# Optimization experiments

Hardware: AMD Instinct MI355X
Metric: run time of the kernel (lower is better)

The kernel has to match this reference:

```python
import jax, jax.numpy as jnp
import numpy as np

N = 131072  # B*L nodes
H = 256     # hidden_dim


def setup_inputs() -> dict:
    key = jax.random.key(0)
    ks = jax.random.split(key, 13)
    s = 0.02
    return {
        "h": jax.random.normal(ks[0], (N, H), jnp.float32),
        "pos": jax.random.normal(ks[1], (N, 3), jnp.float32),
        # edge_mlp: Linear(2H+1 -> H), SiLU, Linear(H -> H)
        "ew1": jax.random.normal(ks[2], (2 * H + 1, H), jnp.float32) * s,
        "eb1": jnp.zeros((H,), jnp.float32),
        "ew2": jax.random.normal(ks[3], (H, H), jnp.float32) * s,
        "eb2": jnp.zeros((H,), jnp.float32),
        # pos_mlp: Linear(H -> H), SiLU, Linear(H -> 3, bias=False)
        "pw1": jax.random.normal(ks[4], (H, H), jnp.float32) * s,
        "pb1": jnp.zeros((H,), jnp.float32),
        "pw2": jax.random.normal(ks[5], (H, 3), jnp.float32) * s,
        # node_mlp: Linear(2H -> H), SiLU, Linear(H -> H)
        "nw1": jax.random.normal(ks[6], (2 * H, H), jnp.float32) * s,
        "nb1": jnp.zeros((H,), jnp.float32),
        "nw2": jax.random.normal(ks[7], (H, H), jnp.float32) * s,
        "nb2": jnp.zeros((H,), jnp.float32),
    }


def reference(h, pos, ew1, eb1, ew2, eb2, pw1, pb1, pw2, nw1, nb1, nw2, nb2):
    # Chain edges: row = 0..N-2, col = 1..N-1 -> slices instead of gathers.
    rel_pos = pos[1:] - pos[:-1]                                   # [N-1, 3]
    dist = jnp.linalg.norm(rel_pos, axis=-1, keepdims=True)        # [N-1, 1]
    edge_feat = jnp.concatenate([h[:-1], h[1:], dist], axis=-1)    # [N-1, 2H+1]
    edge_attr = jax.nn.silu(edge_feat @ ew1 + eb1) @ ew2 + eb2     # [N-1, H]
    delta_pos = jax.nn.silu(edge_attr @ pw1 + pb1) @ pw2           # [N-1, 3]

    hd = h.shape[1]
    z3 = jnp.zeros((1, 3), pos.dtype)
    zH = jnp.zeros((1, hd), h.dtype)
    # scatter-add over unique chain indices == padded shifts
    pos_update = jnp.concatenate([delta_pos, z3], 0) - jnp.concatenate([z3, delta_pos], 0)
    node_update = jnp.concatenate([edge_attr, zH], 0) + jnp.concatenate([zH, edge_attr], 0)

    h_cat = jnp.concatenate([h, node_update], axis=-1)             # [N, 2H]
    h_out = jax.nn.silu(h_cat @ nw1 + nb1) @ nw2 + nb2             # [N, H]
    pos_out = pos + 0.1 * pos_update                               # [N, 3]
    return h_out, pos_out
```

## Files before the change

kernel.cpp:

```cpp
#include <hip/hip_runtime.h>
#include <hip/hip_bf16.h>
#include <math.h>

#define NN 131072
#define HD 256

typedef __bf16 bf16;
typedef __attribute__((ext_vector_type(8))) __bf16 bf16x8;
typedef __attribute__((ext_vector_type(4))) __bf16 bf16x4;
typedef __attribute__((ext_vector_type(4))) float f32x4;

__device__ __forceinline__ float silu_f(float x) { return x / (1.f + __expf(-x)); }

__device__ __forceinline__ float bfu2f(unsigned int lo16) {
    unsigned int u = lo16 << 16;
    return __builtin_bit_cast(float, u);
}
__device__ __forceinline__ unsigned short f2bfu(float f) {
    bf16 b = (bf16)f;
    return __builtin_bit_cast(unsigned short, b);
}

template<int KSTEPS, int RN>
__device__ __forceinline__ void mm_tileR(const bf16* Xl, int bk0, const bf16x8* __restrict__ Bp,
                                         int wave, int lane, f32x4 acc[RN][4]) {
    const int lrow = lane & 15, lkhi = lane >> 4;
    #pragma unroll
    for (int ks = 0; ks < KSTEPS; ++ks) {
        bf16x8 a[RN];
        #pragma unroll
        for (int r = 0; r < RN; ++r)
            a[r] = *(const bf16x8*)&Xl[(r * 16 + lrow) * 264 + ks * 32 + lkhi * 8];
        #pragma unroll
        for (int c = 0; c < 4; ++c) {
            bf16x8 b = Bp[((bk0 + ks) * 16 + wave * 4 + c) * 64 + lane];
            #pragma unroll
            for (int r = 0; r < RN; ++r)
                acc[r][c] = __builtin_amdgcn_mfma_f32_16x16x32_bf16(a[r], b, acc[r][c], 0, 0, 0);
        }
    }
}

__device__ __forceinline__ void packW(const float* __restrict__ W, bf16* __restrict__ P, int idx) {
    int j  = idx & 7;
    int ln = (idx >> 3) & 63;
    int cb = (idx >> 9) & 15;
    int ks = idx >> 13;
    int k = ks * 32 + ((ln >> 4) << 3) + j;
    int n = (cb << 4) + (ln & 15);
    P[idx] = (bf16)W[k * HD + n];
}

__global__ void pack_kernel(const float* __restrict__ ew1, const float* __restrict__ ew2,
                            const float* __restrict__ pw1, const float* __restrict__ nw1,
                            const float* __restrict__ nw2,
                            bf16* __restrict__ ew1p, bf16* __restrict__ ew2p,
                            bf16* __restrict__ pw1p, bf16* __restrict__ nw1p,
                            bf16* __restrict__ nw2p) {
    int t = blockIdx.x * 256 + threadIdx.x;
    if (t < 131072) { packW(ew1, ew1p, t); return; }
    t -= 131072;
    if (t < 65536)  { packW(ew2, ew2p, t); return; }
    t -= 65536;
    if (t < 65536)  { packW(pw1, pw1p, t); return; }
    t -= 65536;
    if (t < 131072) { packW(nw1, nw1p, t); return; }
    t -= 131072;
    if (t < 65536)  { packW(nw2, nw2p, t); return; }
}

__global__ __launch_bounds__(256, 2) void edge_kernel(
    const float* __restrict__ h, const float* __restrict__ pos,
    const float* __restrict__ ew1, const float* __restrict__ eb1,
    const float* __restrict__ eb2, const float* __restrict__ pb1,
    const float* __restrict__ pw2,
    const bf16x8* __restrict__ ew1p, const bf16x8* __restrict__ ew2p,
    const bf16x8* __restrict__ pw1p, const bf16x8* __restrict__ nw1p,
    bf16* __restrict__ q1_g, uint2* __restrict__ p1_g,
    float* __restrict__ dp_g) {
    __shared__ bf16 X[129 * 264];
    __shared__ float dist_s[128];
    __shared__ float dp_s[4][128][3];

    const int tid = threadIdx.x;
    const int lane = tid & 63, wave = tid >> 6;
    const int lrow = lane & 15, lkhi = lane >> 4;
    const int e0 = blockIdx.x * 128;

    for (int idx = tid; idx < 129 * 64; idx += 256) {
        int r = idx >> 6, c4 = (idx & 63) << 2;
        int gr = e0 + r;
        float4 v = make_float4(0.f, 0.f, 0.f, 0.f);
        if (gr < NN) v = *(const float4*)&h[(size_t)gr * HD + c4];
        bf16x4 b;
        b[0] = (bf16)v.x; b[1] = (bf16)v.y; b[2] = (bf16)v.z; b[3] = (bf16)v.w;
        *(bf16x4*)&X[r * 264 + c4] = b;
    }
    if (tid < 128) {
        int e = e0 + tid;
        float d = 0.f;
        if (e < NN - 1) {
            float dx = pos[3 * e + 3] - pos[3 * e];
            float dy = pos[3 * e + 4] - pos[3 * e + 1];
            float dz = pos[3 * e + 5] - pos[3 * e + 2];
            d = sqrtf(dx * dx + dy * dy + dz * dz);
        }
        dist_s[tid] = d;
    }
    float bias1[4], bias2[4], bias3[4], wlast[4], w2l[4][3], b1n[4];
    #pragma unroll
    for (int c = 0; c < 4; ++c) {
        int col = (wave * 4 + c) * 16 + lrow;
        bias1[c] = eb1[col];
        bias2[c] = eb2[col];
        bias3[c] = pb1[col];
        wlast[c] = ew1[512 * HD + col];
        #pragma unroll
        for (int x = 0; x < 3; ++x) w2l[c][x] = pw2[col * 3 + x];
    }
    (void)b1n;
    __syncthreads();

    f32x4 acc[8][4];

    #pragma unroll
    for (int r = 0; r < 8; ++r)
        #pragma unroll
        for (int c = 0; c < 4; ++c) acc[r][c] = (f32x4)0.f;
    mm_tileR<8, 8>(X, 0, nw1p, wave, lane, acc);
    #pragma unroll
    for (int r = 0; r < 8; ++r) {
        size_t nb = (size_t)blockIdx.x * 2 + (r >> 2);
        uint2* p1w = p1_g + (nb * 4 + wave) * 1024;
        #pragma unroll
        for (int c = 0; c < 4; ++c) {
            uint2 v;
            v.x = (unsigned int)f2bfu(acc[r][c][0]) | ((unsigned int)f2bfu(acc[r][c][1]) << 16);
            v.y = (unsigned int)f2bfu(acc[r][c][2]) | ((unsigned int)f2bfu(acc[r][c][3]) << 16);
            p1w[(((r & 3) * 4 + c)) * 64 + lane] = v;
        }
    }

    #pragma unroll
    for (int r = 0; r < 8; ++r)
        #pragma unroll
        for (int c = 0; c < 4; ++c) acc[r][c] = (f32x4)0.f;
    #pragma unroll
    for (int ks = 0; ks < 16; ++ks) {
        const int rb = (ks >= 8) ? 1 : 0;
        const int kk = ks * 32 + lkhi * 8 - rb * 256;
        bf16x8 a[8];
        #pragma unroll
        for (int r = 0; r < 8; ++r)
            a[r] = *(const bf16x8*)&X[(r * 16 + lrow + rb) * 264 + kk];
        #pragma unroll
        for (int c = 0; c < 4; ++c) {
            bf16x8 b = ew1p[(ks * 16 + wave * 4 + c) * 64 + lane];
            #pragma unroll
            for (int r = 0; r < 8; ++r)
                acc[r][c] = __builtin_amdgcn_mfma_f32_16x16x32_bf16(a[r], b, acc[r][c], 0, 0, 0);
        }
    }
    __syncthreads();
    #pragma unroll
    for (int r = 0; r < 8; ++r)
        #pragma unroll
        for (int c = 0; c < 4; ++c)
            #pragma unroll
            for (int q = 0; q < 4; ++q) {
                int row = r * 16 + lkhi * 4 + q;
                int col = (wave * 4 + c) * 16 + lrow;
                float v = acc[r][c][q] + dist_s[row] * wlast[c] + bias1[c];
                X[row * 264 + col] = (bf16)silu_f(v);
            }
    __syncthreads();

    #pragma unroll
    for (int r = 0; r < 8; ++r)
        #pragma unroll
        for (int c = 0; c < 4; ++c) acc[r][c] = (f32x4)0.f;
    mm_tileR<8, 8>(X, 0, ew2p, wave, lane, acc);
    __syncthreads();
    #pragma unroll
    for (int r = 0; r < 8; ++r)
        #pragma unroll
        for (int c = 0; c < 4; ++c)
            #pragma unroll
            for (int q = 0; q < 4; ++q) {
                int row = r * 16 + lkhi * 4 + q;
                int col = (wave * 4 + c) * 16 + lrow;
                X[row * 264 + col] = (bf16)(acc[r][c][q] + bias2[c]);
            }
    __syncthreads();

    #pragma unroll
    for (int r = 0; r < 8; ++r)
        #pragma unroll
        for (int c = 0; c < 4; ++c) acc[r][c] = (f32x4)0.f;
    mm_tileR<8, 8>(X, 0, pw1p, wave, lane, acc);
    #pragma unroll
    for (int r = 0; r < 8; ++r) {
        float red[12];
        #pragma unroll
        for (int q = 0; q < 4; ++q) {
            float t3v[4];
            #pragma unroll
            for (int c = 0; c < 4; ++c) t3v[c] = silu_f(acc[r][c][q] + bias3[c]);
            #pragma unroll
            for (int x = 0; x < 3; ++x) {
                float s = 0.f;
                #pragma unroll
                for (int c = 0; c < 4; ++c) s += t3v[c] * w2l[c][x];
                red[q * 3 + x] = s;
            }
        }
        #pragma unroll
        for (int i = 0; i < 12; ++i) {
            float v = red[i];
            v += __shfl_xor(v, 1);
            v += __shfl_xor(v, 2);
            v += __shfl_xor(v, 4);
            v += __shfl_xor(v, 8);
            red[i] = v;
        }
        if (lrow == 0) {
            #pragma unroll
            for (int q = 0; q < 4; ++q)
                #pragma unroll
                for (int x = 0; x < 3; ++x)
                    dp_s[wave][r * 16 + lkhi * 4 + q][x] = red[q * 3 + x];
        }
    }

    #pragma unroll
    for (int r = 0; r < 8; ++r)
        #pragma unroll
        for (int c = 0; c < 4; ++c) acc[r][c] = (f32x4)0.f;
    mm_tileR<8, 8>(X, 8, nw1p, wave, lane, acc);

    __syncthreads();
    #pragma unroll
    for (int r = 0; r < 8; ++r)
        #pragma unroll
        for (int c = 0; c < 4; ++c)
            #pragma unroll
            for (int q = 0; q < 4; ++q) {
                int row = r * 16 + lkhi * 4 + q;
                int col = (wave * 4 + c) * 16 + lrow;
                X[row * 264 + col] = (bf16)acc[r][c][q];
            }
    for (int idx = tid; idx < 128 * 3; idx += 256) {
        int row = idx / 3, x = idx - row * 3;
        float s = dp_s[0][row][x] + dp_s[1][row][x] + dp_s[2][row][x] + dp_s[3][row][x];
        dp_g[(size_t)(e0 + row) * 3 + x] = s;
    }
    __syncthreads();
    for (int idx = tid; idx < 128 * 128; idx += 256) {
        int r = idx >> 7, cu = idx & 127;
        ((unsigned int*)&q1_g[(size_t)(e0 + r) * HD])[cu] = ((const unsigned int*)&X[r * 264])[cu];
    }
}

__global__ __launch_bounds__(256, 4) void node_kernel(
    const float* __restrict__ pos,
    const float* __restrict__ nb1, const float* __restrict__ nb2,
    const bf16x8* __restrict__ nw2p,
    const bf16* __restrict__ q1_g, const uint2* __restrict__ p1_g,
    const float* __restrict__ dp_g,
    float* __restrict__ h_out, float* __restrict__ pos_out) {
    __shared__ bf16 X[65 * 264];

    const int tid = threadIdx.x;
    const int lane = tid & 63, wave = tid >> 6;
    const int lrow = lane & 15, lkhi = lane >> 4;
    const int n0 = blockIdx.x * 64;

    if (tid < 192) {
        int row = tid & 63, col = tid >> 6;
        int i = n0 + row;
        float dpi = (i < NN - 1) ? dp_g[(size_t)i * 3 + col] : 0.f;
        float dpm = (i > 0) ? dp_g[(size_t)(i - 1) * 3 + col] : 0.f;
        pos_out[(size_t)i * 3 + col] = pos[(size_t)i * 3 + col] + 0.1f * (dpi - dpm);
    }

    for (int idx = tid; idx < 65 * 32; idx += 256) {
        int t = idx >> 5, cu = idx & 31;
        int er = n0 - 1 + t;
        uint4 v = make_uint4(0u, 0u, 0u, 0u);
        if (er >= 0 && er <= NN - 2) v = ((const uint4*)&q1_g[(size_t)er * HD])[cu];
        ((uint4*)&X[t * 264])[cu] = v;
    }
    uint2 p1r[16];
    {
        const uint2* p1p = p1_g + ((size_t)blockIdx.x * 4 + wave) * 1024;
        #pragma unroll
        for (int i = 0; i < 16; ++i) p1r[i] = p1p[i * 64 + lane];
    }
    float b1[4];
    #pragma unroll
    for (int c = 0; c < 4; ++c) b1[c] = nb1[(wave * 4 + c) * 16 + lrow];
    __syncthreads();

    unsigned int t4p[32];
    #pragma unroll
    for (int r = 0; r < 4; ++r)
        #pragma unroll
        for (int c = 0; c < 4; ++c) {
            int i = r * 4 + c;
            int col = (wave * 4 + c) * 16 + lrow;
            #pragma unroll
            for (int qh = 0; qh < 2; ++qh) {
                unsigned int pk = qh == 0 ? p1r[i].x : p1r[i].y;
                unsigned int outp = 0;
                #pragma unroll
                for (int j = 0; j < 2; ++j) {
                    int q = 2 * qh + j;
                    int row = r * 16 + lkhi * 4 + q;
                    float p1v = bfu2f(j == 0 ? (pk & 0xffffu) : (pk >> 16));
                    float z = p1v + (float)X[(row + 1) * 264 + col] + (float)X[row * 264 + col] + b1[c];
                    unsigned short tb = f2bfu(silu_f(z));
                    outp |= (unsigned int)tb << (16 * j);
                }
                t4p[i * 2 + qh] = outp;
            }
        }
    __syncthreads();
    #pragma unroll
    for (int r = 0; r < 4; ++r)
        #pragma unroll
        for (int c = 0; c < 4; ++c) {
            int i = r * 4 + c;
            int col = (wave * 4 + c) * 16 + lrow;
            #pragma unroll
            for (int q = 0; q < 4; ++q) {
                int row = r * 16 + lkhi * 4 + q;
                unsigned int pk = t4p[i * 2 + (q >> 1)];
                unsigned short tb = (unsigned short)((q & 1) ? (pk >> 16) : (pk & 0xffffu));
                X[row * 264 + col] = __builtin_bit_cast(bf16, tb);
            }
        }
    __syncthreads();

    f32x4 acc[4][4];
    #pragma unroll
    for (int r = 0; r < 4; ++r)
        #pragma unroll
        for (int c = 0; c < 4; ++c) acc[r][c] = (f32x4)0.f;
    mm_tileR<8, 4>(X, 0, nw2p, wave, lane, acc);
    float b2[4];
    #pragma unroll
    for (int c = 0; c < 4; ++c) b2[c] = nb2[(wave * 4 + c) * 16 + lrow];
    #pragma unroll
    for (int r = 0; r < 4; ++r)
        #pragma unroll
        for (int c = 0; c < 4; ++c)
            #pragma unroll
            for (int q = 0; q < 4; ++q) {
                int row = r * 16 + lkhi * 4 + q;
                int col = (wave * 4 + c) * 16 + lrow;
                h_out[(size_t)(n0 + row) * HD + col] = acc[r][c][q] + b2[c];
            }
}

extern "C" void kernel_launch(void* const* d_in, const int* in_sizes, int n_in,
                              void* d_out, int out_size, void* d_ws, size_t ws_size,
                              hipStream_t stream) {
    const float* h   = (const float*)d_in[0];
    const float* pos = (const float*)d_in[1];
    const float* ew1 = (const float*)d_in[2];
    const float* eb1 = (const float*)d_in[3];
    const float* ew2 = (const float*)d_in[4];
    const float* eb2 = (const float*)d_in[5];
    const float* pw1 = (const float*)d_in[6];
    const float* pb1 = (const float*)d_in[7];
    const float* pw2 = (const float*)d_in[8];
    const float* nw1 = (const float*)d_in[9];
    const float* nb1 = (const float*)d_in[10];
    const float* nw2 = (const float*)d_in[11];
    const float* nb2 = (const float*)d_in[12];

    char* ws = (char*)d_ws;
    bf16*  q1   = (bf16*)ws;
    float* dp   = (float*)(ws + 67108864);
    uint2* p1   = (uint2*)(ws + 68681728);
    char*  wsw = ws + 135790592;
    bf16*  ew1p = (bf16*)(wsw);
    bf16*  ew2p = (bf16*)(wsw + 262144);
    bf16*  pw1p = (bf16*)(wsw + 393216);
    bf16*  nw1p = (bf16*)(wsw + 524288);
    bf16*  nw2p = (bf16*)(wsw + 786432);

    float* out = (float*)d_out;
    float* h_out = out;
    float* pos_out = out + (size_t)NN * HD;

    pack_kernel<<<1792, 256, 0, stream>>>(ew1, ew2, pw1, nw1, nw2,
                                          ew1p, ew2p, pw1p, nw1p, nw2p);
    edge_kernel<<<1024, 256, 0, stream>>>(h, pos, ew1, eb1, eb2, pb1, pw2,
                                          (const bf16x8*)ew1p, (const bf16x8*)ew2p,
                                          (const bf16x8*)pw1p, (const bf16x8*)nw1p,
                                          q1, p1, dp);
    node_kernel<<<2048, 256, 0, stream>>>(pos, nb1, nb2,
                                          (const bf16x8*)nw2p,
                                          q1, (const uint2*)p1, dp, h_out, pos_out);
}
```

Measured before the change: 278.9 us.

## Fold biases and dist into extra MFMA k-step, prefetch weights, write q1 in fragment layout

Biases and the distance column are packed as extra K rows of the weight matrices, and a ones/dist vector in shared memory feeds one extra MFMA step, so the scalar bias and dist epilogue arithmetic goes away. Weight fragments are double-buffered one k-step ahead to hide global load latency. Some GEMMs swap their A/B operands so each lane's accumulator holds four consecutive columns, which allows packed 8-byte LDS stores. The q1 intermediate is written straight from registers in fragment layout instead of through shared memory, and the node kernel reads it back per lane including a halo row from the previous block. This adds more complex indexing, an extra MFMA step per GEMM, and bias rounding to bf16.

After: 276.5 us. Within noise of the previous version (-0.9%).

```diff
diff --git a/kernel.cpp b/kernel.cpp
--- a/kernel.cpp
+++ b/kernel.cpp
@@ -20,66 +20,111 @@
     bf16 b = (bf16)f;
     return __builtin_bit_cast(unsigned short, b);
 }
-
-template<int KSTEPS, int RN>
-__device__ __forceinline__ void mm_tileR(const bf16* Xl, int bk0, const bf16x8* __restrict__ Bp,
-                                         int wave, int lane, f32x4 acc[RN][4]) {
+__device__ __forceinline__ uint2 pack4(float a, float b, float c, float d) {
+    uint2 v;
+    v.x = (unsigned int)f2bfu(a) | ((unsigned int)f2bfu(b) << 16);
+    v.y = (unsigned int)f2bfu(c) | ((unsigned int)f2bfu(d) << 16);
+    return v;
+}
+
+template<int KS, bool SWAP>
+__device__ __forceinline__ void mmP(const bf16* Xl, int bk0, const bf16x8* __restrict__ Bp,
+                                    int wave, int lane, f32x4 acc[8][4]) {
     const int lrow = lane & 15, lkhi = lane >> 4;
-    #pragma unroll
-    for (int ks = 0; ks < KSTEPS; ++ks) {
-        bf16x8 a[RN];
-        #pragma unroll
-        for (int r = 0; r < RN; ++r)
+    bf16x8 bcur[4], bnxt[4];
+    #pragma unroll
+    for (int c = 0; c < 4; ++c)
+        bcur[c] = Bp[(bk0 * 16 + wave * 4 + c) * 64 + lane];
+    #pragma unroll
+    for (int ks = 0; ks < KS; ++ks) {
+        if (ks + 1 < KS) {
+            #pragma unroll
+            for (int c = 0; c < 4; ++c)
+                bnxt[c] = Bp[((bk0 + ks + 1) * 16 + wave * 4 + c) * 64 + lane];
+        }
+        bf16x8 a[8];
+        #pragma unroll
+        for (int r = 0; r < 8; ++r)
             a[r] = *(const bf16x8*)&Xl[(r * 16 + lrow) * 264 + ks * 32 + lkhi * 8];
         #pragma unroll
-        for (int c = 0; c < 4; ++c) {
-            bf16x8 b = Bp[((bk0 + ks) * 16 + wave * 4 + c) * 64 + lane];
-            #pragma unroll
-            for (int r = 0; r < RN; ++r)
-                acc[r][c] = __builtin_amdgcn_mfma_f32_16x16x32_bf16(a[r], b, acc[r][c], 0, 0, 0);
-        }
-    }
-}
-
-__device__ __forceinline__ void packW(const float* __restrict__ W, bf16* __restrict__ P, int idx) {
+        for (int c = 0; c < 4; ++c)
+            #pragma unroll
+            for (int r = 0; r < 8; ++r)
+                acc[r][c] = SWAP
+                    ? __builtin_amdgcn_mfma_f32_16x16x32_bf16(bcur[c], a[r], acc[r][c], 0, 0, 0)
+                    : __builtin_amdgcn_mfma_f32_16x16x32_bf16(a[r], bcur[c], acc[r][c], 0, 0, 0);
+        #pragma unroll
+        for (int c = 0; c < 4; ++c) bcur[c] = bnxt[c];
+    }
+}
+
+template<bool SWAP>
+__device__ __forceinline__ void extrasStep(const bf16* EXT, const bf16x8* __restrict__ Bp, int ksx,
+                                           int wave, int lane, f32x4 acc[8][4]) {
+    const int lrow = lane & 15, lkhi = lane >> 4;
+    bf16x8 bext[4];
+    #pragma unroll
+    for (int c = 0; c < 4; ++c)
+        bext[c] = Bp[(ksx * 16 + wave * 4 + c) * 64 + lane];
+    bf16x8 zero;
+    #pragma unroll
+    for (int j = 0; j < 8; ++j) zero[j] = (bf16)0.f;
+    #pragma unroll
+    for (int r = 0; r < 8; ++r) {
+        bf16x8 ae = (lkhi == 0) ? *(const bf16x8*)&EXT[(r * 16 + lrow) * 8] : zero;
+        #pragma unroll
+        for (int c = 0; c < 4; ++c)
+            acc[r][c] = SWAP
+                ? __builtin_amdgcn_mfma_f32_16x16x32_bf16(bext[c], ae, acc[r][c], 0, 0, 0)
+                : __builtin_amdgcn_mfma_f32_16x16x32_bf16(ae, bext[c], acc[r][c], 0, 0, 0);
+    }
+}
+
+__device__ __forceinline__ void packGen(const float* __restrict__ W, const float* __restrict__ bias,
+                                        const float* __restrict__ extra, int Kreal,
+                                        bf16* __restrict__ P, int idx) {
     int j  = idx & 7;
     int ln = (idx >> 3) & 63;
     int cb = (idx >> 9) & 15;
     int ks = idx >> 13;
     int k = ks * 32 + ((ln >> 4) << 3) + j;
     int n = (cb << 4) + (ln & 15);
-    P[idx] = (bf16)W[k * HD + n];
-}
-
-__global__ void pack_kernel(const float* __restrict__ ew1, const float* __restrict__ ew2,
-                            const float* __restrict__ pw1, const float* __restrict__ nw1,
-                            const float* __restrict__ nw2,
+    float v;
+    if (k < Kreal) v = W[k * HD + n];
+    else if (k == Kreal) v = bias ? bias[n] : 0.f;
+    else if (k == Kreal + 1) v = extra ? extra[n] : 0.f;
+    else v = 0.f;
+    P[idx] = (bf16)v;
+}
+
+__global__ void pack_kernel(const float* __restrict__ ew1, const float* __restrict__ eb1,
+                            const float* __restrict__ ew2, const float* __restrict__ eb2,
+                            const float* __restrict__ pw1, const float* __restrict__ pb1,
+                            const float* __restrict__ nw1, const float* __restrict__ nw2,
                             bf16* __restrict__ ew1p, bf16* __restrict__ ew2p,
                             bf16* __restrict__ pw1p, bf16* __restrict__ nw1p,
                             bf16* __restrict__ nw2p) {
     int t = blockIdx.x * 256 + threadIdx.x;
-    if (t < 131072) { packW(ew1, ew1p, t); return; }
+    if (t < 139264) { packGen(ew1, eb1, ew1 + 512 * HD, 512, ew1p, t); return; }
+    t -= 139264;
+    if (t < 73728)  { packGen(ew2, eb2, nullptr, 256, ew2p, t); return; }
+    t -= 73728;
+    if (t < 73728)  { packGen(pw1, pb1, nullptr, 256, pw1p, t); return; }
+    t -= 73728;
+    if (t < 131072) { packGen(nw1, nullptr, nullptr, 512, nw1p, t); return; }
     t -= 131072;
-    if (t < 65536)  { packW(ew2, ew2p, t); return; }
-    t -= 65536;
-    if (t < 65536)  { packW(pw1, pw1p, t); return; }
-    t -= 65536;
-    if (t < 131072) { packW(nw1, nw1p, t); return; }
-    t -= 131072;
-    if (t < 65536)  { packW(nw2, nw2p, t); return; }
+    if (t < 65536)  { packGen(nw2, nullptr, nullptr, 256, nw2p, t); return; }
 }
 
 __global__ __launch_bounds__(256, 2) void edge_kernel(
     const float* __restrict__ h, const float* __restrict__ pos,
-    const float* __restrict__ ew1, const float* __restrict__ eb1,
-    const float* __restrict__ eb2, const float* __restrict__ pb1,
     const float* __restrict__ pw2,
     const bf16x8* __restrict__ ew1p, const bf16x8* __restrict__ ew2p,
     const bf16x8* __restrict__ pw1p, const bf16x8* __restrict__ nw1p,
-    bf16* __restrict__ q1_g, uint2* __restrict__ p1_g,
+    uint2* __restrict__ q1f_g, uint2* __restrict__ p1_g,
     float* __restrict__ dp_g) {
     __shared__ bf16 X[129 * 264];
-    __shared__ float dist_s[128];
+    __shared__ bf16 EXT[128 * 8];
     __shared__ float dp_s[4][128][3];
 
     const int tid = threadIdx.x;
@@ -105,20 +150,19 @@
             float dz = pos[3 * e + 5] - pos[3 * e + 2];
             d = sqrtf(dx * dx + dy * dy + dz * dz);
         }
-        dist_s[tid] = d;
-    }
-    float bias1[4], bias2[4], bias3[4], wlast[4], w2l[4][3], b1n[4];
+        uint2 a, z;
+        a.x = (unsigned int)f2bfu(1.0f) | ((unsigned int)f2bfu(d) << 16);
+        a.y = 0u; z.x = 0u; z.y = 0u;
+        *(uint2*)&EXT[tid * 8] = a;
+        *(uint2*)&EXT[tid * 8 + 4] = z;
+    }
+    float w2l[4][3];
     #pragma unroll
     for (int c = 0; c < 4; ++c) {
-        int col = (wave * 4 + c) * 16 + lrow;
-        bias1[c] = eb1[col];
-        bias2[c] = eb2[col];
-        bias3[c] = pb1[col];
-        wlast[c] = ew1[512 * HD + col];
-        #pragma unroll
-        for (int x = 0; x < 3; ++x) w2l[c][x] = pw2[col * 3 + x];
-    }
-    (void)b1n;
+        int n = (wave * 4 + c) * 16 + lrow;
+        #pragma unroll
+        for (int x = 0; x < 3; ++x) w2l[c][x] = pw2[n * 3 + x];
+    }
     __syncthreads();
 
     f32x4 acc[8][4];
@@ -127,77 +171,86 @@
     for (int r = 0; r < 8; ++r)
         #pragma unroll
         for (int c = 0; c < 4; ++c) acc[r][c] = (f32x4)0.f;
-    mm_tileR<8, 8>(X, 0, nw1p, wave, lane, acc);
+    mmP<8, true>(X, 0, nw1p, wave, lane, acc);
     #pragma unroll
     for (int r = 0; r < 8; ++r) {
         size_t nb = (size_t)blockIdx.x * 2 + (r >> 2);
-        uint2* p1w = p1_g + (nb * 4 + wave) * 1024;
+        uint2* w = p1_g + (nb * 4 + wave) * 1024;
+        #pragma unroll
+        for (int c = 0; c < 4; ++c)
+            w[((r & 3) * 4 + c) * 64 + lane] =
+                pack4(acc[r][c][0], acc[r][c][1], acc[r][c][2], acc[r][c][3]);
+    }
+
+    #pragma unroll
+    for (int r = 0; r < 8; ++r)
+        #pragma unroll
+        for (int c = 0; c < 4; ++c) acc[r][c] = (f32x4)0.f;
+    {
+        bf16x8 bcur[4], bnxt[4];
+        #pragma unroll
+        for (int c = 0; c < 4; ++c)
+            bcur[c] = ew1p[(wave * 4 + c) * 64 + lane];
+        #pragma unroll
+        for (int ks = 0; ks < 16; ++ks) {
+            if (ks < 15) {
+                #pragma unroll
+                for (int c = 0; c < 4; ++c)
+                    bnxt[c] = ew1p[((ks + 1) * 16 + wave * 4 + c) * 64 + lane];
+            }
+            const int rb = (ks >= 8) ? 1 : 0;
+            const int kk = ks * 32 + lkhi * 8 - rb * 256;
+            bf16x8 a[8];
+            #pragma unroll
+            for (int r = 0; r < 8; ++r)
+                a[r] = *(const bf16x8*)&X[(r * 16 + lrow + rb) * 264 + kk];
+            #pragma unroll
+            for (int c = 0; c < 4; ++c)
+                #pragma unroll
+                for (int r = 0; r < 8; ++r)
+                    acc[r][c] = __builtin_amdgcn_mfma_f32_16x16x32_bf16(bcur[c], a[r], acc[r][c], 0, 0, 0);
+            #pragma unroll
+            for (int c = 0; c < 4; ++c) bcur[c] = bnxt[c];
+        }
+    }
+    extrasStep<true>(EXT, ew1p, 16, wave, lane, acc);
+    __syncthreads();
+    #pragma unroll
+    for (int r = 0; r < 8; ++r)
         #pragma unroll
         for (int c = 0; c < 4; ++c) {
-            uint2 v;
-            v.x = (unsigned int)f2bfu(acc[r][c][0]) | ((unsigned int)f2bfu(acc[r][c][1]) << 16);
-            v.y = (unsigned int)f2bfu(acc[r][c][2]) | ((unsigned int)f2bfu(acc[r][c][3]) << 16);
-            p1w[(((r & 3) * 4 + c)) * 64 + lane] = v;
-        }
-    }
-
-    #pragma unroll
-    for (int r = 0; r < 8; ++r)
-        #pragma unroll
-        for (int c = 0; c < 4; ++c) acc[r][c] = (f32x4)0.f;
-    #pragma unroll
-    for (int ks = 0; ks < 16; ++ks) {
-        const int rb = (ks >= 8) ? 1 : 0;
-        const int kk = ks * 32 + lkhi * 8 - rb * 256;
-        bf16x8 a[8];
-        #pragma unroll
-        for (int r = 0; r < 8; ++r)
-            a[r] = *(const bf16x8*)&X[(r * 16 + lrow + rb) * 264 + kk];
+            int m = 16 * r + lrow;
+            int col0 = (wave * 4 + c) * 16 + 4 * lkhi;
+            *(uint2*)&X[m * 264 + col0] =
+                pack4(silu_f(acc[r][c][0]), silu_f(acc[r][c][1]),
+                      silu_f(acc[r][c][2]), silu_f(acc[r][c][3]));
+        }
+    __syncthreads();
+
+    #pragma unroll
+    for (int r = 0; r < 8; ++r)
+        #pragma unroll
+        for (int c = 0; c < 4; ++c) acc[r][c] = (f32x4)0.f;
+    mmP<8, true>(X, 0, ew2p, wave, lane, acc);
+    extrasStep<true>(EXT, ew2p, 8, wave, lane, acc);
+    __syncthreads();
+    #pragma unroll
+    for (int r = 0; r < 8; ++r)
         #pragma unroll
         for (int c = 0; c < 4; ++c) {
-            bf16x8 b = ew1p[(ks * 16 + wave * 4 + c) * 64 + lane];
-            #pragma unroll
-            for (int r = 0; r < 8; ++r)
-                acc[r][c] = __builtin_amdgcn_mfma_f32_16x16x32_bf16(a[r], b, acc[r][c], 0, 0, 0);
-        }
-    }
-    __syncthreads();
-    #pragma unroll
-    for (int r = 0; r < 8; ++r)
-        #pragma unroll
-        for (int c = 0; c < 4; ++c)
-            #pragma unroll
-            for (int q = 0; q < 4; ++q) {
-                int row = r * 16 + lkhi * 4 + q;
-                int col = (wave * 4 + c) * 16 + lrow;
-                float v = acc[r][c][q] + dist_s[row] * wlast[c] + bias1[c];
-                X[row * 264 + col] = (bf16)silu_f(v);
-            }
-    __syncthreads();
-
-    #pragma unroll
-    for (int r = 0; r < 8; ++r)
-        #pragma unroll
-        for (int c = 0; c < 4; ++c) acc[r][c] = (f32x4)0.f;
-    mm_tileR<8, 8>(X, 0, ew2p, wave, lane, acc);
-    __syncthreads();
-    #pragma unroll
-    for (int r = 0; r < 8; ++r)
-        #pragma unroll
-        for (int c = 0; c < 4; ++c)
-            #pragma unroll
-            for (int q = 0; q < 4; ++q) {
-                int row = r * 16 + lkhi * 4 + q;
-                int col = (wave * 4 + c) * 16 + lrow;
-                X[row * 264 + col] = (bf16)(acc[r][c][q] + bias2[c]);
-            }
-    __syncthreads();
-
-    #pragma unroll
-    for (int r = 0; r < 8; ++r)
-        #pragma unroll
-        for (int c = 0; c < 4; ++c) acc[r][c] = (f32x4)0.f;
-    mm_tileR<8, 8>(X, 0, pw1p, wave, lane, acc);
+            int m = 16 * r + lrow;
+            int col0 = (wave * 4 + c) * 16 + 4 * lkhi;
+            *(uint2*)&X[m * 264 + col0] =
+                pack4(acc[r][c][0], acc[r][c][1], acc[r][c][2], acc[r][c][3]);
+        }
+    __syncthreads();
+
+    #pragma unroll
+    for (int r = 0; r < 8; ++r)
+        #pragma unroll
+        for (int c = 0; c < 4; ++c) acc[r][c] = (f32x4)0.f;
+    mmP<8, false>(X, 0, pw1p, wave, lane, acc);
+    extrasStep<false>(EXT, pw1p, 8, wave, lane, acc);
     #pragma unroll
     for (int r = 0; r < 8; ++r) {
         float red[12];
@@ -205,7 +258,7 @@
         for (int q = 0; q < 4; ++q) {
             float t3v[4];
             #pragma unroll
-            for (int c = 0; c < 4; ++c) t3v[c] = silu_f(acc[r][c][q] + bias3[c]);
+            for (int c = 0; c < 4; ++c) t3v[c] = silu_f(acc[r][c][q]);
             #pragma unroll
             for (int x = 0; x < 3; ++x) {
                 float s = 0.f;
@@ -228,36 +281,30 @@
             for (int q = 0; q < 4; ++q)
                 #pragma unroll
                 for (int x = 0; x < 3; ++x)
-                    dp_s[wave][r * 16 + lkhi * 4 + q][x] = red[q * 3 + x];
-        }
-    }
-
-    #pragma unroll
-    for (int r = 0; r < 8; ++r)
-        #pragma unroll
-        for (int c = 0; c < 4; ++c) acc[r][c] = (f32x4)0.f;
-    mm_tileR<8, 8>(X, 8, nw1p, wave, lane, acc);
-
-    __syncthreads();
-    #pragma unroll
-    for (int r = 0; r < 8; ++r)
-        #pragma unroll
-        for (int c = 0; c < 4; ++c)
-            #pragma unroll
-            for (int q = 0; q < 4; ++q) {
-                int row = r * 16 + lkhi * 4 + q;
-                int col = (wave * 4 + c) * 16 + lrow;
-                X[row * 264 + col] = (bf16)acc[r][c][q];
-            }
-    for (int idx = tid; idx < 128 * 3; idx += 256) {
+                    dp_s[wave][16 * r + 4 * lkhi + q][x] = red[q * 3 + x];
+        }
+    }
+
+    #pragma unroll
+    for (int r = 0; r < 8; ++r)
+        #pragma unroll
+        for (int c = 0; c < 4; ++c) acc[r][c] = (f32x4)0.f;
+    mmP<8, true>(X, 8, nw1p, wave, lane, acc);
+    #pragma unroll
+    for (int r = 0; r < 8; ++r) {
+        size_t nb = (size_t)blockIdx.x * 2 + (r >> 2);
+        uint2* w = q1f_g + (nb * 4 + wave) * 1024;
+        #pragma unroll
+        for (int c = 0; c < 4; ++c)
+            w[((r & 3) * 4 + c) * 64 + lane] =
+                pack4(acc[r][c][0], acc[r][c][1], acc[r][c][2], acc[r][c][3]);
+    }
+
+    __syncthreads();
+    for (int idx = tid; idx < 384; idx += 256) {
         int row = idx / 3, x = idx - row * 3;
-        float s = dp_s[0][row][x] + dp_s[1][row][x] + dp_s[2][row][x] + dp_s[3][row][x];
-        dp_g[(size_t)(e0 + row) * 3 + x] = s;
-    }
-    __syncthreads();
-    for (int idx = tid; idx < 128 * 128; idx += 256) {
-        int r = idx >> 7, cu = idx & 127;
-        ((unsigned int*)&q1_g[(size_t)(e0 + r) * HD])[cu] = ((const unsigned int*)&X[r * 264])[cu];
+        dp_g[(size_t)(e0 + row) * 3 + x] =
+            dp_s[0][row][x] + dp_s[1][row][x] + dp_s[2][row][x] + dp_s[3][row][x];
     }
 }
 
@@ -265,7 +312,7 @@
     const float* __restrict__ pos,
     const float* __restrict__ nb1, const float* __restrict__ nb2,
     const bf16x8* __restrict__ nw2p,
-    const bf16* __restrict__ q1_g, const uint2* __restrict__ p1_g,
+    const uint2* __restrict__ q1f_g, const uint2* __restrict__ p1_g,
     const float* __restrict__ dp_g,
     float* __restrict__ h_out, float* __restrict__ pos_out) {
     __shared__ bf16 X[65 * 264];
@@ -283,70 +330,92 @@
         pos_out[(size_t)i * 3 + col] = pos[(size_t)i * 3 + col] + 0.1f * (dpi - dpm);
     }
 
-    for (int idx = tid; idx < 65 * 32; idx += 256) {
-        int t = idx >> 5, cu = idx & 31;
-        int er = n0 - 1 + t;
-        uint4 v = make_uint4(0u, 0u, 0u, 0u);
-        if (er >= 0 && er <= NN - 2) v = ((const uint4*)&q1_g[(size_t)er * HD])[cu];
-        ((uint4*)&X[t * 264])[cu] = v;
-    }
     uint2 p1r[16];
     {
-        const uint2* p1p = p1_g + ((size_t)blockIdx.x * 4 + wave) * 1024;
-        #pragma unroll
-        for (int i = 0; i < 16; ++i) p1r[i] = p1p[i * 64 + lane];
-    }
-    float b1[4];
-    #pragma unroll
-    for (int c = 0; c < 4; ++c) b1[c] = nb1[(wave * 4 + c) * 16 + lrow];
-    __syncthreads();
-
-    unsigned int t4p[32];
+        const uint2* pp = p1_g + ((size_t)blockIdx.x * 4 + wave) * 1024;
+        #pragma unroll
+        for (int i = 0; i < 16; ++i) p1r[i] = pp[i * 64 + lane];
+    }
+    {
+        const uint2* qp = q1f_g + ((size_t)blockIdx.x * 4 + wave) * 1024;
+        #pragma unroll
+        for (int i = 0; i < 16; ++i) {
+            uint2 v = qp[i * 64 + lane];
+            int m = 16 * (i >> 2) + lrow;
+            if (n0 + m > NN - 2) { v.x = 0u; v.y = 0u; }
+            int col0 = (wave * 4 + (i & 3)) * 16 + 4 * lkhi;
+            *(uint2*)&X[(m + 1) * 264 + col0] = v;
+        }
+    }
+    if (lrow == 0) {
+        #pragma unroll
+        for (int c = 0; c < 4; ++c) {
+            uint2 v; v.x = 0u; v.y = 0u;
+            if (blockIdx.x > 0)
+                v = q1f_g[((size_t)(blockIdx.x - 1) * 4 + wave) * 1024 + (12 + c) * 64 + (15 + 16 * lkhi)];
+            *(uint2*)&X[(wave * 4 + c) * 16 + 4 * lkhi] = v;
+        }
+    }
+    float4 b1v[4];
+    #pragma unroll
+    for (int c = 0; c < 4; ++c)
+        b1v[c] = *(const float4*)&nb1[(wave * 4 + c) * 16 + 4 * lkhi];
+    __syncthreads();
+
+    uint2 t4p[16];
+    #pragma unroll
+    for (int i = 0; i < 16; ++i) {
+        int m = 16 * (i >> 2) + lrow;
+        int col0 = (wave * 4 + (i & 3)) * 16 + 4 * lkhi;
+        uint2 qm1 = *(const uint2*)&X[m * 264 + col0];
+        uint2 qm  = *(const uint2*)&X[(m + 1) * 264 + col0];
+        uint2 p = p1r[i];
+        float4 bb = b1v[i & 3];
+        float z0 = bfu2f(p.x & 0xffffu) + bfu2f(qm.x & 0xffffu) + bfu2f(qm1.x & 0xffffu) + bb.x;
+        float z1 = bfu2f(p.x >> 16)     + bfu2f(qm.x >> 16)     + bfu2f(qm1.x >> 16)     + bb.y;
+        float z2 = bfu2f(p.y & 0xffffu) + bfu2f(qm.y & 0xffffu) + bfu2f(qm1.y & 0xffffu) + bb.z;
+        float z3 = bfu2f(p.y >> 16)     + bfu2f(qm.y >> 16)     + bfu2f(qm1.y >> 16)     + bb.w;
+        t4p[i] = pack4(silu_f(z0), silu_f(z1), silu_f(z2), silu_f(z3));
+    }
+    __syncthreads();
+    #pragma unroll
+    for (int i = 0; i < 16; ++i) {
+        int m = 16 * (i >> 2) + lrow;
+        int col0 = (wave * 4 + (i & 3)) * 16 + 4 * lkhi;
+        *(uint2*)&X[m * 264 + col0] = t4p[i];
+    }
+    __syncthreads();
+
+    f32x4 acc[4][4];
     #pragma unroll
     for (int r = 0; r < 4; ++r)
         #pragma unroll
-        for (int c = 0; c < 4; ++c) {
-            int i = r * 4 + c;
-            int col = (wave * 4 + c) * 16 + lrow;
-            #pragma unroll
-            for (int qh = 0; qh < 2; ++qh) {
-                unsigned int pk = qh == 0 ? p1r[i].x : p1r[i].y;
-                unsigned int outp = 0;
-                #pragma unroll
-                for (int j = 0; j < 2; ++j) {
-                    int q = 2 * qh + j;
-                    int row = r * 16 + lkhi * 4 + q;
-                    float p1v = bfu2f(j == 0 ? (pk & 0xffffu) : (pk >> 16));
-                    float z = p1v + (float)X[(row + 1) * 264 + col] + (float)X[row * 264 + col] + b1[c];
-                    unsigned short tb = f2bfu(silu_f(z));
-                    outp |= (unsigned int)tb << (16 * j);
-                }
-                t4p[i * 2 + qh] = outp;
+        for (int c = 0; c < 4; ++c) acc[r][c] = (f32x4)0.f;
+    {
+        bf16x8 bcur[4], bnxt[4];
+        #pragma unroll
+        for (int c = 0; c < 4; ++c)
+            bcur[c] = nw2p[(wave * 4 + c) * 64 + lane];
+        #pragma unroll
+        for (int ks = 0; ks < 8; ++ks) {
+            if (ks < 7) {
+                #pragma unroll
+                for (int c = 0; c < 4; ++c)
+                    bnxt[c] = nw2p[((ks + 1) * 16 + wave * 4 + c) * 64 + lane];
             }
-        }
-    __syncthreads();
-    #pragma unroll
-    for (int r = 0; r < 4; ++r)
-        #pragma unroll
-        for (int c = 0; c < 4; ++c) {
-            int i = r * 4 + c;
-            int col = (wave * 4 + c) * 16 + lrow;
-            #pragma unroll
-            for (int q = 0; q < 4; ++q) {
-                int row = r * 16 + lkhi * 4 + q;
-                unsigned int pk = t4p[i * 2 + (q >> 1)];
-                unsigned short tb = (unsigned short)((q & 1) ? (pk >> 16) : (pk & 0xffffu));
-                X[row * 264 + col] = __builtin_bit_cast(bf16, tb);
-            }
-        }
-    __syncthreads();
-
-    f32x4 acc[4][4];
-    #pragma unroll
-    for (int r = 0; r < 4; ++r)
-        #pragma unroll
-        for (int c = 0; c < 4; ++c) acc[r][c] = (f32x4)0.f;
-    mm_tileR<8, 4>(X, 0, nw2p, wave, lane, acc);
+            bf16x8 a[4];
+            #pragma unroll
+            for (int r = 0; r < 4; ++r)
+                a[r] = *(const bf16x8*)&X[(r * 16 + lrow) * 264 + ks * 32 + lkhi * 8];
+            #pragma unroll
+            for (int c = 0; c < 4; ++c)
+                #pragma unroll
+                for (int r = 0; r < 4; ++r)
+                    acc[r][c] = __builtin_amdgcn_mfma_f32_16x16x32_bf16(a[r], bcur[c], acc[r][c], 0, 0, 0);
+            #pragma unroll
+            for (int c = 0; c < 4; ++c) bcur[c] = bnxt[c];
+        }
+    }
     float b2[4];
     #pragma unroll
     for (int c = 0; c < 4; ++c) b2[c] = nb2[(wave * 4 + c) * 16 + lrow];
@@ -380,27 +449,28 @@
     const float* nb2 = (const float*)d_in[12];
 
     char* ws = (char*)d_ws;
-    bf16*  q1   = (bf16*)ws;
+    uint2* q1f  = (uint2*)ws;
     float* dp   = (float*)(ws + 67108864);
     uint2* p1   = (uint2*)(ws + 68681728);
     char*  wsw = ws + 135790592;
     bf16*  ew1p = (bf16*)(wsw);
-    bf16*  ew2p = (bf16*)(wsw + 262144);
-    bf16*  pw1p = (bf16*)(wsw + 393216);
-    bf16*  nw1p = (bf16*)(wsw + 524288);
-    bf16*  nw2p = (bf16*)(wsw + 786432);
+    bf16*  ew2p = (bf16*)(wsw + 278528);
+    bf16*  pw1p = (bf16*)(wsw + 425984);
+    bf16*  nw1p = (bf16*)(wsw + 573440);
+    bf16*  nw2p = (bf16*)(wsw + 835584);
 
     float* out = (float*)d_out;
     float* h_out = out;
     float* pos_out = out + (size_t)NN * HD;
 
-    pack_kernel<<<1792, 256, 0, stream>>>(ew1, ew2, pw1, nw1, nw2,
+    pack_kernel<<<1888, 256, 0, stream>>>(ew1, eb1, ew2, eb2, pw1, pb1, nw1, nw2,
                                           ew1p, ew2p, pw1p, nw1p, nw2p);
-    edge_kernel<<<1024, 256, 0, stream>>>(h, pos, ew1, eb1, eb2, pb1, pw2,
+    edge_kernel<<<1024, 256, 0, stream>>>(h, pos, pw2,
                                           (const bf16x8*)ew1p, (const bf16x8*)ew2p,
                                           (const bf16x8*)pw1p, (const bf16x8*)nw1p,
-                                          q1, p1, dp);
+                                          q1f, p1, dp);
     node_kernel<<<2048, 256, 0, stream>>>(pos, nb1, nb2,
                                           (const bf16x8*)nw2p,
-                                          q1, (const uint2*)p1, dp, h_out, pos_out);
-}
+                                          (const uint2*)q1f, (const uint2*)p1, dp,
+                                          h_out, pos_out);
+}
```
